# Performance work log

Measured on AMD Instinct MI355X. Metric: run time of the kernel, lower is better.

## Reference

```python
import jax, jax.numpy as jnp
import numpy as np
from jax import lax

V, H, A, S = 256, 2048, 512, 512  # vocab, hidden, attn, seq_len


def setup_inputs() -> dict:
    key = jax.random.key(0)
    ks = jax.random.split(key, 8)
    sc = 0.02  # small init to keep tanh unsaturated
    return {
        "x_enc": jax.random.normal(ks[0], (S, V), jnp.float32),
        "x_dec": jax.random.normal(ks[1], (S, V), jnp.float32),
        "W_enc": jax.random.normal(ks[2], (H, V + H), jnp.float32) * sc,
        "b_enc": jnp.zeros((H,), jnp.float32),
        "Wa_enc": jax.random.normal(ks[3], (A, H), jnp.float32) * sc,
        "Wa_dec": jax.random.normal(ks[4], (A, H), jnp.float32) * sc,
        "v_a": jax.random.normal(ks[5], (A,), jnp.float32) * sc,
        "W_dec": jax.random.normal(ks[6], (H, V + 2 * H), jnp.float32) * sc,
        "b_dec": jnp.zeros((H,), jnp.float32),
        "W_out": jax.random.normal(ks[7], (V, H), jnp.float32) * sc,
        "b_out": jnp.zeros((V,), jnp.float32),
    }


def reference(x_enc, x_dec, W_enc, b_enc, Wa_enc, Wa_dec, v_a, W_dec, b_dec, W_out, b_out):
    h0 = jnp.zeros((W_enc.shape[0],), x_enc.dtype)

    # Encoder: h_t = tanh(W_enc [x_t ; h_{t-1}] + b)
    def enc_step(h, x):
        h_new = jnp.tanh(jnp.concatenate([x, h]) @ W_enc.T + b_enc)
        return h_new, h_new

    h_enc, enc_states = lax.scan(enc_step, h0, x_enc)  # enc_states: (S, H)

    # Encoder-side attention projection is step-invariant -> hoist (same math).
    enc_proj = enc_states @ Wa_enc.T  # (S, A)

    # Decoder with per-step Bahdanau additive attention.
    def dec_step(h, x):
        dec_proj = h @ Wa_dec.T                              # (A,)
        energy = jnp.tanh(enc_proj + dec_proj) @ v_a         # (S,)
        attn_w = jax.nn.softmax(energy)                      # (S,)
        context = attn_w @ enc_states                        # (H,)
        h_new = jnp.tanh(jnp.concatenate([x, context, h]) @ W_dec.T + b_dec)
        logits = h_new @ W_out.T + b_out                     # (V,)
        return h_new, logits

    _, outputs = lax.scan(dec_step, h_enc, x_dec)  # (S, V)
    return outputs
```

## Files before the change

kernel.cpp:

```cpp
#include <hip/hip_runtime.h>

#define V 256
#define H 2048
#define A 512
#define S 512
#define NBLK 128
#define NTHR 512
#define CH 64
#define HPH (512*CH)
#define DPH (128*CH)
#define SENTU 0x7FC00000u
#define SENT64 0x7FC000007FC00000ULL

typedef float f32x4 __attribute__((ext_vector_type(4)));
typedef float f32x2 __attribute__((ext_vector_type(2)));
typedef unsigned long long u64;

__device__ __forceinline__ f32x4 ld_cg4(const float* p) {
    f32x4 r;
    asm volatile("global_load_dwordx4 %0, %1, off sc0 sc1\n\ts_waitcnt vmcnt(0)"
                 : "=&v"(r) : "v"(p) : "memory");
    return r;
}
__device__ __forceinline__ f32x4 poll4(const float* p) {
    f32x4 r = ld_cg4(p);
    while (__float_as_uint(r.x) == SENTU || __float_as_uint(r.y) == SENTU ||
           __float_as_uint(r.z) == SENTU || __float_as_uint(r.w) == SENTU)
        r = ld_cg4(p);
    return r;
}

__device__ __forceinline__ void vm_drain() { asm volatile("s_waitcnt vmcnt(0)" ::: "memory"); }
__device__ __forceinline__ void ax_st64(u64* p, u64 v) {
    (void)__hip_atomic_exchange(p, v, __ATOMIC_RELAXED, __HIP_MEMORY_SCOPE_AGENT);
}
__device__ __forceinline__ void ax_st32(unsigned* p, unsigned v) {
    (void)__hip_atomic_exchange(p, v, __ATOMIC_RELAXED, __HIP_MEMORY_SCOPE_AGENT);
}
__device__ __forceinline__ u64 pack2(float a, float b) {
    return ((u64)__float_as_uint(b) << 32) | (u64)__float_as_uint(a);
}

__device__ __forceinline__ void st_rst2(float* p) {
    f32x2 v; v.x = __uint_as_float(SENTU); v.y = __uint_as_float(SENTU);
    asm volatile("global_store_dwordx2 %0, %1, off sc0 sc1" :: "v"(p), "v"(v) : "memory");
}
__device__ __forceinline__ void st_rst1(float* p) {
    float v = __uint_as_float(SENTU);
    asm volatile("global_store_dword %0, %1, off sc0 sc1" :: "v"(p), "v"(v) : "memory");
}

__global__ void init_ex(unsigned* p, int n) {
    int i = blockIdx.x * blockDim.x + threadIdx.x;
    if (i < n) p[i] = SENTU;
}

__global__ __launch_bounds__(256) void gemm_nt(
    const float* __restrict__ Amat, int lda,
    const float* __restrict__ Bmat, int ldb,
    float* __restrict__ C, int ldc,
    const float* __restrict__ bias, int M, int N, int K)
{
    __shared__ float As[16][68];
    __shared__ float Bs[16][68];
    const int tid = threadIdx.x;
    const int tx = tid & 15;
    const int ty = tid >> 4;
    const int m0 = blockIdx.y * 64;
    const int n0 = blockIdx.x * 64;
    const int lr = tid >> 2;
    const int lk = (tid & 3) * 4;

    float acc[4][4] = {};
    for (int k0 = 0; k0 < K; k0 += 16) {
        float4 av = *(const float4*)(Amat + (size_t)(m0 + lr) * lda + k0 + lk);
        float4 bv = *(const float4*)(Bmat + (size_t)(n0 + lr) * ldb + k0 + lk);
        __syncthreads();
        As[lk+0][lr] = av.x; As[lk+1][lr] = av.y; As[lk+2][lr] = av.z; As[lk+3][lr] = av.w;
        Bs[lk+0][lr] = bv.x; Bs[lk+1][lr] = bv.y; Bs[lk+2][lr] = bv.z; Bs[lk+3][lr] = bv.w;
        __syncthreads();
        #pragma unroll
        for (int k = 0; k < 16; ++k) {
            float a4[4], b4[4];
            #pragma unroll
            for (int i = 0; i < 4; ++i) a4[i] = As[k][ty*4+i];
            #pragma unroll
            for (int j = 0; j < 4; ++j) b4[j] = Bs[k][tx*4+j];
            #pragma unroll
            for (int i = 0; i < 4; ++i)
                #pragma unroll
                for (int j = 0; j < 4; ++j) acc[i][j] += a4[i] * b4[j];
        }
    }
    #pragma unroll
    for (int i = 0; i < 4; ++i) {
        const int m = m0 + ty*4 + i;
        #pragma unroll
        for (int j = 0; j < 4; ++j) {
            const int n = n0 + tx*4 + j;
            float v = acc[i][j];
            if (bias) v += bias[n];
            C[(size_t)m * ldc + n] = v;
        }
    }
}

__global__ __launch_bounds__(NTHR, 2) void enc_scan(
    const float* __restrict__ W_enc, const float* __restrict__ accx,
    float* __restrict__ states, float* __restrict__ hex)
{
    __shared__ __align__(16) float hs[2][H];
    const int tid = threadIdx.x;
    const int wid = tid >> 6, lane = tid & 63;
    const int w   = blockIdx.x * 8 + wid;
    const int r0  = 2*w, r1 = r0 + 1;
    const int slot = (w >> 1)*CH + (w & 1)*2;

    f32x4 we0[8], we1[8];
    #pragma unroll
    for (int k = 0; k < 8; ++k) {
        we0[k] = *(const f32x4*)(W_enc + (size_t)r0*(V+H) + V + 4*(lane + 64*k));
        we1[k] = *(const f32x4*)(W_enc + (size_t)r1*(V+H) + V + 4*(lane + 64*k));
    }

    if (lane == 0) {
        float h0 = tanhf(accx[r0]), h1 = tanhf(accx[r1]);
        vm_drain();
        ax_st64((u64*)(hex + 0*HPH + slot), pack2(h0, h1));
        states[r0] = h0; states[r1] = h1;
    }

    for (int t = 1; t < S; ++t) {
        float ax0 = accx[(size_t)t*H + r0];
        float ax1 = accx[(size_t)t*H + r1];
        ((f32x4*)hs[t&1])[tid] = poll4(hex + ((t-1)%3)*HPH + tid*CH);
        __syncthreads();
        if (lane == 0) st_rst2(hex + ((t+1)%3)*HPH + slot);

        const f32x4* h4 = (const f32x4*)hs[t&1];
        float a0 = 0.f, a1 = 0.f;
        #pragma unroll
        for (int k = 0; k < 8; ++k) {
            f32x4 hv = h4[lane + 64*k];
            a0 += we0[k].x*hv.x + we0[k].y*hv.y + we0[k].z*hv.z + we0[k].w*hv.w;
            a1 += we1[k].x*hv.x + we1[k].y*hv.y + we1[k].z*hv.z + we1[k].w*hv.w;
        }
        #pragma unroll
        for (int off = 32; off; off >>= 1) { a0 += __shfl_down(a0, off); a1 += __shfl_down(a1, off); }
        if (lane == 0) {
            float h0 = tanhf(a0 + ax0);
            float h1 = tanhf(a1 + ax1);
            vm_drain();
            ax_st64((u64*)(hex + (t%3)*HPH + slot), pack2(h0, h1));
            states[(size_t)t*H + r0] = h0;
            states[(size_t)t*H + r1] = h1;
        }
    }
}

__global__ __launch_bounds__(NTHR, 2) void dec_scan(
    const float* __restrict__ Wa_dec, const float* __restrict__ W_dec,
    const float* __restrict__ enc_proj, const float* __restrict__ v_a,
    const float* __restrict__ WcT, const float* __restrict__ accx,
    const float* __restrict__ enc_states, float* __restrict__ h_dec,
    float* __restrict__ hexd, float* __restrict__ dpex, float* __restrict__ eex)
{
    __shared__ __align__(16) float hs[2][H];
    __shared__ __align__(16) float ps[A];
    __shared__ __align__(16) float es[S];
    __shared__ float zred[8];
    const int tid = threadIdx.x;
    const int wid = tid >> 6, lane = tid & 63;
    const int w   = blockIdx.x * 8 + wid;
    const int r0  = 2*w, r1 = r0 + 1;
    const int hslot = (w >> 1)*CH + (w & 1)*2;
    const bool attn = ((w & 1) == 0);
    const int s_row = w >> 1;
    const int aslot = (s_row >> 2)*CH + (s_row & 3);

    f32x4 wh0[8], wh1[8], wa[8], wc0[2], wc1[2], ep[2], va[2];
    #pragma unroll
    for (int k = 0; k < 8; ++k) {
        wh0[k] = *(const f32x4*)(W_dec + (size_t)r0*(V+2*H) + V + H + 4*(lane + 64*k));
        wh1[k] = *(const f32x4*)(W_dec + (size_t)r1*(V+2*H) + V + H + 4*(lane + 64*k));
        wa[k]  = (f32x4)(0.f);
    }
    #pragma unroll
    for (int k = 0; k < 2; ++k) {
        wc0[k] = *(const f32x4*)(WcT + (size_t)r0*S + 4*(lane + 64*k));
        wc1[k] = *(const f32x4*)(WcT + (size_t)r1*S + 4*(lane + 64*k));
        ep[k] = (f32x4)(0.f); va[k] = (f32x4)(0.f);
    }
    if (attn) {
        #pragma unroll
        for (int k = 0; k < 8; ++k)
            wa[k] = *(const f32x4*)(Wa_dec + (size_t)s_row*H + 4*(lane + 64*k));
        #pragma unroll
        for (int k = 0; k < 2; ++k) {
            ep[k] = *(const f32x4*)(enc_proj + (size_t)s_row*A + 4*(lane + 64*k));
            va[k] = *(const f32x4*)(v_a + 4*(lane + 64*k));
        }
    }
    const f32x4* ps4 = (const f32x4*)ps;
    const f32x4* es4 = (const f32x4*)es;

    for (int t = 0; t < S; ++t) {
        const int ph  = t % 3;
        const int phn = (t+1) % 3;
        const int php = (t+2) % 3;

        float ax0 = accx[(size_t)t*H + r0];
        float ax1 = accx[(size_t)t*H + r1];

        if (t == 0) ((f32x4*)hs[0])[tid] = ((const f32x4*)(enc_states + (size_t)(S-1)*H))[tid];
        else        ((f32x4*)hs[t&1])[tid] = poll4(hexd + php*HPH + tid*CH);
        __syncthreads();

        if (lane == 0) st_rst2(hexd + phn*HPH + hslot);
        if (t > 0 && attn && lane == 0) {
            st_rst1(dpex + php*DPH + aslot);
            st_rst1(eex  + php*DPH + aslot);
        }

        const f32x4* h4 = (const f32x4*)hs[t&1];

        if (attn) {
            float aP = 0.f;
            #pragma unroll
            for (int k = 0; k < 8; ++k) {
                f32x4 hv = h4[lane + 64*k];
                aP += wa[k].x*hv.x + wa[k].y*hv.y + wa[k].z*hv.z + wa[k].w*hv.w;
            }
            #pragma unroll
            for (int off = 32; off; off >>= 1) aP += __shfl_down(aP, off);
            if (lane == 0) {
                vm_drain();
                ax_st32((unsigned*)(dpex + ph*DPH + aslot), __float_as_uint(aP));
            }
        }
        float aH0 = 0.f, aH1 = 0.f;
        #pragma unroll
        for (int k = 0; k < 8; ++k) {
            f32x4 hv = h4[lane + 64*k];
            aH0 += wh0[k].x*hv.x + wh0[k].y*hv.y + wh0[k].z*hv.z + wh0[k].w*hv.w;
            aH1 += wh1[k].x*hv.x + wh1[k].y*hv.y + wh1[k].z*hv.z + wh1[k].w*hv.w;
        }
        #pragma unroll
        for (int off = 32; off; off >>= 1) { aH0 += __shfl_down(aH0, off); aH1 += __shfl_down(aH1, off); }

        if (tid < 128) ((f32x4*)ps)[tid] = poll4(dpex + ph*DPH + tid*CH);
        __syncthreads();
        if (attn) {
            float e_ = 0.f;
            #pragma unroll
            for (int k = 0; k < 2; ++k) {
                f32x4 p = ps4[lane + 64*k];
                e_ += va[k].x*tanhf(ep[k].x + p.x) + va[k].y*tanhf(ep[k].y + p.y)
                    + va[k].z*tanhf(ep[k].z + p.z) + va[k].w*tanhf(ep[k].w + p.w);
            }
            #pragma unroll
            for (int off = 32; off; off >>= 1) e_ += __shfl_down(e_, off);
            if (lane == 0) {
                vm_drain();
                ax_st32((unsigned*)(eex + ph*DPH + aslot), __float_as_uint(expf(e_)));
            }
        }

        if (tid < 128) ((f32x4*)es)[tid] = poll4(eex + ph*DPH + tid*CH);
        __syncthreads();

        float z = es[tid];
        #pragma unroll
        for (int off = 32; off; off >>= 1) z += __shfl_down(z, off);
        if (lane == 0) zred[wid] = z;
        __syncthreads();
        const float Z = zred[0]+zred[1]+zred[2]+zred[3]+zred[4]+zred[5]+zred[6]+zred[7];

        float c0 = 0.f, c1 = 0.f;
        #pragma unroll
        for (int k = 0; k < 2; ++k) {
            f32x4 ev = es4[lane + 64*k];
            c0 += wc0[k].x*ev.x + wc0[k].y*ev.y + wc0[k].z*ev.z + wc0[k].w*ev.w;
            c1 += wc1[k].x*ev.x + wc1[k].y*ev.y + wc1[k].z*ev.z + wc1[k].w*ev.w;
        }
        #pragma unroll
        for (int off = 32; off; off >>= 1) { c0 += __shfl_down(c0, off); c1 += __shfl_down(c1, off); }

        if (lane == 0) {
            const float Zi = 1.f / Z;
            float h0 = tanhf(ax0 + aH0 + c0*Zi);
            float h1 = tanhf(ax1 + aH1 + c1*Zi);
            vm_drain();
            ax_st64((u64*)(hexd + ph*HPH + hslot), pack2(h0, h1));
            f32x2 hv; hv.x = h0; hv.y = h1;
            *(f32x2*)(h_dec + (size_t)t*H + r0) = hv;
        }
    }
}

extern "C" void kernel_launch(void* const* d_in, const int* in_sizes, int n_in,
                              void* d_out, int out_size, void* d_ws, size_t ws_size,
                              hipStream_t stream) {
    const float* x_enc  = (const float*)d_in[0];
    const float* x_dec  = (const float*)d_in[1];
    const float* W_enc  = (const float*)d_in[2];
    const float* b_enc  = (const float*)d_in[3];
    const float* Wa_enc = (const float*)d_in[4];
    const float* Wa_dec = (const float*)d_in[5];
    const float* v_a    = (const float*)d_in[6];
    const float* W_dec  = (const float*)d_in[7];
    const float* b_dec  = (const float*)d_in[8];
    const float* W_out  = (const float*)d_in[9];
    const float* b_out  = (const float*)d_in[10];
    float* out = (float*)d_out;

    float* ws         = (float*)d_ws;
    float* accx_enc   = ws;
    float* enc_states = accx_enc + (size_t)S*H;
    float* enc_proj   = enc_states + (size_t)S*H;
    float* WcT        = enc_proj + (size_t)S*A;
    float* accx_dec   = WcT + (size_t)H*S;
    float* h_dec      = accx_dec + (size_t)S*H;
    float* hex_e      = h_dec + (size_t)S*H;
    float* hex_d      = hex_e + 3*HPH;
    float* dp_ex      = hex_d + 3*HPH;
    float* e_ex       = dp_ex + 3*DPH;
    const int n_ex = 3*HPH*2 + 3*DPH*2;

    dim3 b256(256);

    init_ex<<<dim3((n_ex + 255)/256), b256, 0, stream>>>((unsigned*)hex_e, n_ex);

    gemm_nt<<<dim3(H/64, S/64), b256, 0, stream>>>(x_enc, V, W_enc, V+H, accx_enc, H, b_enc, S, H, V);
    gemm_nt<<<dim3(H/64, S/64), b256, 0, stream>>>(x_dec, V, W_dec, V+2*H, accx_dec, H, b_dec, S, H, V);

    {
        const float* We = W_enc; const float* ax = accx_enc; float* st = enc_states; float* hx = hex_e;
        void* args[] = { &We, &ax, &st, &hx };
        hipLaunchCooperativeKernel((void*)enc_scan, dim3(NBLK), dim3(NTHR), args, 0, stream);
    }

    gemm_nt<<<dim3(A/64, S/64), b256, 0, stream>>>(enc_states, H, Wa_enc, H, enc_proj, A, nullptr, S, A, H);
    gemm_nt<<<dim3(S/64, H/64), b256, 0, stream>>>(W_dec + V, V+2*H, enc_states, H, WcT, S, nullptr, H, S, H);

    {
        const float* wa = Wa_dec; const float* wd = W_dec; const float* epj = enc_proj;
        const float* vv = v_a; const float* wc = WcT; const float* ax = accx_dec;
        const float* est = enc_states; float* hd = h_dec;
        float* hx = hex_d; float* dx = dp_ex; float* ex = e_ex;
        void* args[] = { &wa, &wd, &epj, &vv, &wc, &ax, &est, &hd, &hx, &dx, &ex };
        hipLaunchCooperativeKernel((void*)dec_scan, dim3(NBLK), dim3(NTHR), args, 0, stream);
    }

    gemm_nt<<<dim3(V/64, S/64), b256, 0, stream>>>(h_dec, H, W_out, H, out, V, b_out, S, V, H);
}
```

Measured before the change: 6.828 ms.

## Fuse input projections and context-weight GEMM into persistent scan kernels

Removes the two input-projection GEMMs and the W_dec·enc_states GEMM. The x·W contribution is now computed inside each scan step from a per-step x row staged in shared memory. The context weight table is built in the decoder prologue by a 512-step loop over encoder states. Publishing stores also switch from atomic exchange to plain sc0 sc1 stores with a waitcnt, which lowers per-step handoff cost. In exchange, the serial scans do extra per-step work and the decoder prologue adds a long sequential loop with a barrier per step.

```diff
diff --git a/kernel.cpp b/kernel.cpp
--- a/kernel.cpp
+++ b/kernel.cpp
@@ -30,17 +30,22 @@
     return r;
 }
 
+__device__ __forceinline__ void st_pub2(float* p, float x, float y) {
+    f32x2 v; v.x = x; v.y = y;
+    asm volatile("s_waitcnt vmcnt(0)\n\tglobal_store_dwordx2 %0, %1, off sc0 sc1"
+                 :: "v"(p), "v"(v) : "memory");
+}
+__device__ __forceinline__ void st_pub1(float* p, float x) {
+    asm volatile("s_waitcnt vmcnt(0)\n\tglobal_store_dword %0, %1, off sc0 sc1"
+                 :: "v"(p), "v"(x) : "memory");
+}
 __device__ __forceinline__ void vm_drain() { asm volatile("s_waitcnt vmcnt(0)" ::: "memory"); }
 __device__ __forceinline__ void ax_st64(u64* p, u64 v) {
     (void)__hip_atomic_exchange(p, v, __ATOMIC_RELAXED, __HIP_MEMORY_SCOPE_AGENT);
 }
-__device__ __forceinline__ void ax_st32(unsigned* p, unsigned v) {
-    (void)__hip_atomic_exchange(p, v, __ATOMIC_RELAXED, __HIP_MEMORY_SCOPE_AGENT);
-}
 __device__ __forceinline__ u64 pack2(float a, float b) {
     return ((u64)__float_as_uint(b) << 32) | (u64)__float_as_uint(a);
 }
-
 __device__ __forceinline__ void st_rst2(float* p) {
     f32x2 v; v.x = __uint_as_float(SENTU); v.y = __uint_as_float(SENTU);
     asm volatile("global_store_dwordx2 %0, %1, off sc0 sc1" :: "v"(p), "v"(v) : "memory");
@@ -106,10 +111,12 @@
 }
 
 __global__ __launch_bounds__(NTHR, 2) void enc_scan(
-    const float* __restrict__ W_enc, const float* __restrict__ accx,
+    const float* __restrict__ W_enc, const float* __restrict__ x_enc,
+    const float* __restrict__ b_enc,
     float* __restrict__ states, float* __restrict__ hex)
 {
     __shared__ __align__(16) float hs[2][H];
+    __shared__ __align__(16) float xs[2][V];
     const int tid = threadIdx.x;
     const int wid = tid >> 6, lane = tid & 63;
     const int w   = blockIdx.x * 8 + wid;
@@ -122,23 +129,36 @@
         we0[k] = *(const f32x4*)(W_enc + (size_t)r0*(V+H) + V + 4*(lane + 64*k));
         we1[k] = *(const f32x4*)(W_enc + (size_t)r1*(V+H) + V + 4*(lane + 64*k));
     }
-
-    if (lane == 0) {
-        float h0 = tanhf(accx[r0]), h1 = tanhf(accx[r1]);
-        vm_drain();
-        ax_st64((u64*)(hex + 0*HPH + slot), pack2(h0, h1));
-        states[r0] = h0; states[r1] = h1;
+    const f32x4 wx0 = *(const f32x4*)(W_enc + (size_t)r0*(V+H) + 4*lane);
+    const f32x4 wx1 = *(const f32x4*)(W_enc + (size_t)r1*(V+H) + 4*lane);
+    const float bb0 = b_enc[r0], bb1 = b_enc[r1];
+
+    if (tid < 64) ((f32x4*)xs[0])[tid] = ((const f32x4*)x_enc)[tid];
+    __syncthreads();
+    {
+        f32x4 xv = ((const f32x4*)xs[0])[lane];
+        float a0 = wx0.x*xv.x + wx0.y*xv.y + wx0.z*xv.z + wx0.w*xv.w;
+        float a1 = wx1.x*xv.x + wx1.y*xv.y + wx1.z*xv.z + wx1.w*xv.w;
+        #pragma unroll
+        for (int off = 32; off; off >>= 1) { a0 += __shfl_down(a0, off); a1 += __shfl_down(a1, off); }
+        if (lane == 0) {
+            float h0 = tanhf(a0 + bb0), h1 = tanhf(a1 + bb1);
+            vm_drain();
+            ax_st64((u64*)(hex + 0*HPH + slot), pack2(h0, h1));
+            states[r0] = h0; states[r1] = h1;
+        }
     }
 
     for (int t = 1; t < S; ++t) {
-        float ax0 = accx[(size_t)t*H + r0];
-        float ax1 = accx[(size_t)t*H + r1];
+        if (tid < 64) ((f32x4*)xs[t&1])[tid] = ((const f32x4*)(x_enc + (size_t)t*V))[tid];
         ((f32x4*)hs[t&1])[tid] = poll4(hex + ((t-1)%3)*HPH + tid*CH);
         __syncthreads();
         if (lane == 0) st_rst2(hex + ((t+1)%3)*HPH + slot);
 
+        f32x4 xv = ((const f32x4*)xs[t&1])[lane];
+        float a0 = wx0.x*xv.x + wx0.y*xv.y + wx0.z*xv.z + wx0.w*xv.w;
+        float a1 = wx1.x*xv.x + wx1.y*xv.y + wx1.z*xv.z + wx1.w*xv.w;
         const f32x4* h4 = (const f32x4*)hs[t&1];
-        float a0 = 0.f, a1 = 0.f;
         #pragma unroll
         for (int k = 0; k < 8; ++k) {
             f32x4 hv = h4[lane + 64*k];
@@ -148,8 +168,7 @@
         #pragma unroll
         for (int off = 32; off; off >>= 1) { a0 += __shfl_down(a0, off); a1 += __shfl_down(a1, off); }
         if (lane == 0) {
-            float h0 = tanhf(a0 + ax0);
-            float h1 = tanhf(a1 + ax1);
+            float h0 = tanhf(a0 + bb0), h1 = tanhf(a1 + bb1);
             vm_drain();
             ax_st64((u64*)(hex + (t%3)*HPH + slot), pack2(h0, h1));
             states[(size_t)t*H + r0] = h0;
@@ -161,13 +180,15 @@
 __global__ __launch_bounds__(NTHR, 2) void dec_scan(
     const float* __restrict__ Wa_dec, const float* __restrict__ W_dec,
     const float* __restrict__ enc_proj, const float* __restrict__ v_a,
-    const float* __restrict__ WcT, const float* __restrict__ accx,
+    const float* __restrict__ x_dec, const float* __restrict__ b_dec,
     const float* __restrict__ enc_states, float* __restrict__ h_dec,
     float* __restrict__ hexd, float* __restrict__ dpex, float* __restrict__ eex)
 {
     __shared__ __align__(16) float hs[2][H];
     __shared__ __align__(16) float ps[A];
     __shared__ __align__(16) float es[S];
+    __shared__ __align__(16) float xs[2][V];
+    __shared__ __align__(16) float wct[8][2][S];
     __shared__ float zred[8];
     const int tid = threadIdx.x;
     const int wid = tid >> 6, lane = tid & 63;
@@ -178,7 +199,39 @@
     const int s_row = w >> 1;
     const int aslot = (s_row >> 2)*CH + (s_row & 3);
 
-    f32x4 wh0[8], wh1[8], wa[8], wc0[2], wc1[2], ep[2], va[2];
+    f32x4 wc0[2], wc1[2];
+    {
+        f32x4 wcr0[8], wcr1[8];
+        #pragma unroll
+        for (int k = 0; k < 8; ++k) {
+            wcr0[k] = *(const f32x4*)(W_dec + (size_t)r0*(V+2*H) + V + 4*(lane + 64*k));
+            wcr1[k] = *(const f32x4*)(W_dec + (size_t)r1*(V+2*H) + V + 4*(lane + 64*k));
+        }
+        for (int s = 0; s < S; ++s) {
+            ((f32x4*)hs[s&1])[tid] = ((const f32x4*)(enc_states + (size_t)s*H))[tid];
+            __syncthreads();
+            const f32x4* h4 = (const f32x4*)hs[s&1];
+            float p0 = 0.f, p1 = 0.f;
+            #pragma unroll
+            for (int k = 0; k < 8; ++k) {
+                f32x4 hv = h4[lane + 64*k];
+                p0 += wcr0[k].x*hv.x + wcr0[k].y*hv.y + wcr0[k].z*hv.z + wcr0[k].w*hv.w;
+                p1 += wcr1[k].x*hv.x + wcr1[k].y*hv.y + wcr1[k].z*hv.z + wcr1[k].w*hv.w;
+            }
+            #pragma unroll
+            for (int off = 32; off; off >>= 1) { p0 += __shfl_down(p0, off); p1 += __shfl_down(p1, off); }
+            if (lane == 0) { wct[wid][0][s] = p0; wct[wid][1][s] = p1; }
+        }
+        __syncthreads();
+        #pragma unroll
+        for (int k = 0; k < 2; ++k) {
+            wc0[k] = *(const f32x4*)(&wct[wid][0][4*(lane + 64*k)]);
+            wc1[k] = *(const f32x4*)(&wct[wid][1][4*(lane + 64*k)]);
+        }
+        __syncthreads();
+    }
+
+    f32x4 wh0[8], wh1[8], wa[8], ep[2], va[2];
     #pragma unroll
     for (int k = 0; k < 8; ++k) {
         wh0[k] = *(const f32x4*)(W_dec + (size_t)r0*(V+2*H) + V + H + 4*(lane + 64*k));
@@ -186,11 +239,7 @@
         wa[k]  = (f32x4)(0.f);
     }
     #pragma unroll
-    for (int k = 0; k < 2; ++k) {
-        wc0[k] = *(const f32x4*)(WcT + (size_t)r0*S + 4*(lane + 64*k));
-        wc1[k] = *(const f32x4*)(WcT + (size_t)r1*S + 4*(lane + 64*k));
-        ep[k] = (f32x4)(0.f); va[k] = (f32x4)(0.f);
-    }
+    for (int k = 0; k < 2; ++k) { ep[k] = (f32x4)(0.f); va[k] = (f32x4)(0.f); }
     if (attn) {
         #pragma unroll
         for (int k = 0; k < 8; ++k)
@@ -201,6 +250,10 @@
             va[k] = *(const f32x4*)(v_a + 4*(lane + 64*k));
         }
     }
+    const f32x4 wx0 = *(const f32x4*)(W_dec + (size_t)r0*(V+2*H) + 4*lane);
+    const f32x4 wx1 = *(const f32x4*)(W_dec + (size_t)r1*(V+2*H) + 4*lane);
+    const float bb0 = b_dec[r0], bb1 = b_dec[r1];
+
     const f32x4* ps4 = (const f32x4*)ps;
     const f32x4* es4 = (const f32x4*)es;
 
@@ -209,8 +262,7 @@
         const int phn = (t+1) % 3;
         const int php = (t+2) % 3;
 
-        float ax0 = accx[(size_t)t*H + r0];
-        float ax1 = accx[(size_t)t*H + r1];
+        if (tid < 64) ((f32x4*)xs[t&1])[tid] = ((const f32x4*)(x_dec + (size_t)t*V))[tid];
 
         if (t == 0) ((f32x4*)hs[0])[tid] = ((const f32x4*)(enc_states + (size_t)(S-1)*H))[tid];
         else        ((f32x4*)hs[t&1])[tid] = poll4(hexd + php*HPH + tid*CH);
@@ -233,12 +285,11 @@
             }
             #pragma unroll
             for (int off = 32; off; off >>= 1) aP += __shfl_down(aP, off);
-            if (lane == 0) {
-                vm_drain();
-                ax_st32((unsigned*)(dpex + ph*DPH + aslot), __float_as_uint(aP));
-            }
-        }
-        float aH0 = 0.f, aH1 = 0.f;
+            if (lane == 0) st_pub1(dpex + ph*DPH + aslot, aP);
+        }
+        f32x4 xv = ((const f32x4*)xs[t&1])[lane];
+        float aH0 = wx0.x*xv.x + wx0.y*xv.y + wx0.z*xv.z + wx0.w*xv.w;
+        float aH1 = wx1.x*xv.x + wx1.y*xv.y + wx1.z*xv.z + wx1.w*xv.w;
         #pragma unroll
         for (int k = 0; k < 8; ++k) {
             f32x4 hv = h4[lane + 64*k];
@@ -260,10 +311,7 @@
             }
             #pragma unroll
             for (int off = 32; off; off >>= 1) e_ += __shfl_down(e_, off);
-            if (lane == 0) {
-                vm_drain();
-                ax_st32((unsigned*)(eex + ph*DPH + aslot), __float_as_uint(expf(e_)));
-            }
+            if (lane == 0) st_pub1(eex + ph*DPH + aslot, expf(e_));
         }
 
         if (tid < 128) ((f32x4*)es)[tid] = poll4(eex + ph*DPH + tid*CH);
@@ -288,10 +336,9 @@
 
         if (lane == 0) {
             const float Zi = 1.f / Z;
-            float h0 = tanhf(ax0 + aH0 + c0*Zi);
-            float h1 = tanhf(ax1 + aH1 + c1*Zi);
-            vm_drain();
-            ax_st64((u64*)(hexd + ph*HPH + hslot), pack2(h0, h1));
+            float h0 = tanhf(aH0 + bb0 + c0*Zi);
+            float h1 = tanhf(aH1 + bb1 + c1*Zi);
+            st_pub2(hexd + ph*HPH + hslot, h0, h1);
             f32x2 hv; hv.x = h0; hv.y = h1;
             *(f32x2*)(h_dec + (size_t)t*H + r0) = hv;
         }
@@ -315,12 +362,9 @@
     float* out = (float*)d_out;
 
     float* ws         = (float*)d_ws;
-    float* accx_enc   = ws;
-    float* enc_states = accx_enc + (size_t)S*H;
+    float* enc_states = ws;
     float* enc_proj   = enc_states + (size_t)S*H;
-    float* WcT        = enc_proj + (size_t)S*A;
-    float* accx_dec   = WcT + (size_t)H*S;
-    float* h_dec      = accx_dec + (size_t)S*H;
+    float* h_dec      = enc_proj + (size_t)S*A;
     float* hex_e      = h_dec + (size_t)S*H;
     float* hex_d      = hex_e + 3*HPH;
     float* dp_ex      = hex_d + 3*HPH;
@@ -331,24 +375,21 @@
 
     init_ex<<<dim3((n_ex + 255)/256), b256, 0, stream>>>((unsigned*)hex_e, n_ex);
 
-    gemm_nt<<<dim3(H/64, S/64), b256, 0, stream>>>(x_enc, V, W_enc, V+H, accx_enc, H, b_enc, S, H, V);
-    gemm_nt<<<dim3(H/64, S/64), b256, 0, stream>>>(x_dec, V, W_dec, V+2*H, accx_dec, H, b_dec, S, H, V);
-
     {
-        const float* We = W_enc; const float* ax = accx_enc; float* st = enc_states; float* hx = hex_e;
-        void* args[] = { &We, &ax, &st, &hx };
+        const float* We = W_enc; const float* xe = x_enc; const float* be = b_enc;
+        float* st = enc_states; float* hx = hex_e;
+        void* args[] = { &We, &xe, &be, &st, &hx };
         hipLaunchCooperativeKernel((void*)enc_scan, dim3(NBLK), dim3(NTHR), args, 0, stream);
     }
 
     gemm_nt<<<dim3(A/64, S/64), b256, 0, stream>>>(enc_states, H, Wa_enc, H, enc_proj, A, nullptr, S, A, H);
-    gemm_nt<<<dim3(S/64, H/64), b256, 0, stream>>>(W_dec + V, V+2*H, enc_states, H, WcT, S, nullptr, H, S, H);
 
     {
         const float* wa = Wa_dec; const float* wd = W_dec; const float* epj = enc_proj;
-        const float* vv = v_a; const float* wc = WcT; const float* ax = accx_dec;
+        const float* vv = v_a; const float* xd = x_dec; const float* bd = b_dec;
         const float* est = enc_states; float* hd = h_dec;
         float* hx = hex_d; float* dx = dp_ex; float* ex = e_ex;
-        void* args[] = { &wa, &wd, &epj, &vv, &wc, &ax, &est, &hd, &hx, &dx, &ex };
+        void* args[] = { &wa, &wd, &epj, &vv, &xd, &bd, &est, &hd, &hx, &dx, &ex };
         hipLaunchCooperativeKernel((void*)dec_scan, dim3(NBLK), dim3(NTHR), args, 0, stream);
     }
 
```

Measured after the change: 6.387 ms. -6.5%, faster.
